# Kernel optimization log

Measured on AMD Instinct MI355X. Metric: run time of the kernel, lower is better.

The kernel has to match this reference:

```python
import jax, jax.numpy as jnp
import numpy as np
import math

B, S, D, H, DFF = 2, 2048, 1024, 16, 4096
DK = D // H
EPS = 1e-5


def setup_inputs() -> dict:
    key = jax.random.key(0)
    ks = jax.random.split(key, 8)
    s = 0.02
    return {
        "x": jax.random.normal(ks[0], (B, S, D), jnp.float32),
        "wq": jax.random.normal(ks[1], (D, D), jnp.float32) * s,
        "bq": jnp.zeros((D,), jnp.float32),
        "wk": jax.random.normal(ks[2], (D, D), jnp.float32) * s,
        "bk": jnp.zeros((D,), jnp.float32),
        "wv": jax.random.normal(ks[3], (D, D), jnp.float32) * s,
        "bv": jnp.zeros((D,), jnp.float32),
        "wo": jax.random.normal(ks[4], (D, D), jnp.float32) * s,
        "bo": jnp.zeros((D,), jnp.float32),
        "g1": jnp.ones((D,), jnp.float32),
        "beta1": jnp.zeros((D,), jnp.float32),
        "w1": jax.random.normal(ks[5], (D, DFF), jnp.float32) * s,
        "b1": jnp.zeros((DFF,), jnp.float32),
        "w2": jax.random.normal(ks[6], (DFF, D), jnp.float32) * s,
        "b2": jnp.zeros((D,), jnp.float32),
        "g2": jnp.ones((D,), jnp.float32),
        "beta2": jnp.zeros((D,), jnp.float32),
    }


def _layernorm(x, g, b):
    m = jnp.mean(x, axis=-1, keepdims=True)
    v = jnp.mean(jnp.square(x - m), axis=-1, keepdims=True)
    return (x - m) * jax.lax.rsqrt(v + EPS) * g + b


def reference(x, wq, bq, wk, bk, wv, bv, wo, bo, g1, beta1, w1, b1, w2, b2, g2, beta2):
    b, s, _ = x.shape
    # QKV projections -> [b, h, s, dk]
    q = (x @ wq + bq).reshape(b, s, H, DK).transpose(0, 2, 1, 3)
    k = (x @ wk + bk).reshape(b, s, H, DK).transpose(0, 2, 1, 3)
    v = (x @ wv + bv).reshape(b, s, H, DK).transpose(0, 2, 1, 3)
    scores = jnp.einsum('bhqd,bhkd->bhqk', q, k) / math.sqrt(DK)  # [b,h,s,s]
    # Faithful to source: softmax over dim=1 (heads axis), not the key axis.
    attn = jax.nn.softmax(scores, axis=1)
    ctx = jnp.einsum('bhqk,bhkd->bhqd', attn, v)
    ctx = ctx.transpose(0, 2, 1, 3).reshape(b, s, D)
    attn_out = ctx @ wo + bo
    # dropout is identity in eval mode
    x1 = _layernorm(x + attn_out, g1, beta1)
    ff = jax.nn.relu(x1 @ w1 + b1) @ w2 + b2
    return _layernorm(x1 + ff, g2, beta2)
```

## Files before the change

kernel.cpp:

```cpp
#include <hip/hip_runtime.h>
#include <stdint.h>

#define B_   2
#define S_   2048
#define D_   1024
#define H_   16
#define DK_  64
#define DFF_ 4096
#define M_   (B_ * S_)
#define QKV_LD 3072

typedef unsigned short u16;
typedef unsigned int   u32;
typedef __attribute__((ext_vector_type(8))) short short8;
typedef __attribute__((ext_vector_type(4))) float f32x4;

__device__ __forceinline__ float b2f(u16 u) {
  union { u32 i; float f; } z; z.i = ((u32)u) << 16; return z.f;
}
__device__ __forceinline__ u16 f2b(float f) {
  union { float f; u32 i; } z; z.f = f;
  u32 x = z.i;
  u32 r = (x + 0x7fffu + ((x >> 16) & 1u)) >> 16;
  return (u16)r;
}
__device__ __forceinline__ void load4(const float* p, float* f) {
  float4 v = *(const float4*)p;
  f[0] = v.x; f[1] = v.y; f[2] = v.z; f[3] = v.w;
}
__device__ __forceinline__ void load4(const u16* p, float* f) {
  uint2 v = *(const uint2*)p;
  f[0] = b2f(v.x & 0xffffu); f[1] = b2f(v.x >> 16);
  f[2] = b2f(v.y & 0xffffu); f[3] = b2f(v.y >> 16);
}
__device__ __forceinline__ void tstore(float* p, float v) { *p = v; }
__device__ __forceinline__ void tstore(u16* p, float v)   { *p = f2b(v); }

__device__ __forceinline__ void gld_lds16(const void* g, void* l) {
  __builtin_amdgcn_global_load_lds(
      (const __attribute__((address_space(1))) void*)g,
      (__attribute__((address_space(3))) void*)l, 16, 0, 0);
}

template<int BM, bool RELU, bool RES, bool BIAS, bool QKV, typename TO>
__global__ __launch_bounds__(256)
void gemm_bf16(const u16* __restrict__ A, const u16* __restrict__ Wt,
               const float* __restrict__ bias0, const float* __restrict__ bias1,
               const float* __restrict__ bias2, const float* __restrict__ res,
               TO* __restrict__ C, int M, int N, int K)
{
  constexpr int WM = BM / 2;
  constexpr int MI = WM / 16;
  __shared__ u16 As[BM][32];
  __shared__ u16 Bs[128][32];

  const int tid  = threadIdx.x;
  const int wave = tid >> 6;
  const int lane = tid & 63;
  const int lo16 = lane & 15;
  const int quad = lane >> 4;
  const int row0 = blockIdx.y * BM;
  const int col0 = blockIdx.x * 128;
  const int mb   = (wave & 1) * WM;
  const int nb   = (wave >> 1) * 64;

  const float* bias = bias0;
  float osc = 1.0f;
  if (QKV) {
    const int seg = col0 >> 10;
    bias = (seg == 0) ? bias0 : (seg == 1 ? bias1 : bias2);
    if (seg == 0) osc = 0.125f;
  }
  const int bc0 = QKV ? (col0 & 1023) : col0;

  f32x4 acc[MI][4];
#pragma unroll
  for (int i = 0; i < MI; ++i)
#pragma unroll
    for (int j = 0; j < 4; ++j) acc[i][j] = (f32x4){0.f, 0.f, 0.f, 0.f};

  const int s_row = tid >> 2;
  const int s_ch  = (tid & 3) * 8;
  const u16* gA = A  + (size_t)(row0 + s_row) * K + s_ch;
  const u16* gB = Wt + (size_t)(col0 + s_row) * K + s_ch;

  for (int k0 = 0; k0 < K; k0 += 32) {
    gld_lds16(gA, &As[s_row][s_ch]);
    if constexpr (BM == 128)
      gld_lds16(gA + (size_t)64 * K, &As[s_row + (BM == 128 ? 64 : 0)][s_ch]);
    gld_lds16(gB, &Bs[s_row][s_ch]);
    gld_lds16(gB + (size_t)64 * K, &Bs[s_row + 64][s_ch]);
    gA += 32; gB += 32;
    __syncthreads();

    short8 af[MI], bf[4];
#pragma unroll
    for (int mi = 0; mi < MI; ++mi)
      af[mi] = *(const short8*)&As[mb + mi * 16 + lo16][quad * 8];
#pragma unroll
    for (int ni = 0; ni < 4; ++ni)
      bf[ni] = *(const short8*)&Bs[nb + ni * 16 + lo16][quad * 8];
#pragma unroll
    for (int mi = 0; mi < MI; ++mi)
#pragma unroll
      for (int ni = 0; ni < 4; ++ni)
        acc[mi][ni] = __builtin_amdgcn_mfma_f32_16x16x32_bf16(af[mi], bf[ni], acc[mi][ni], 0, 0, 0);
    __syncthreads();
  }

  float bv[4];
#pragma unroll
  for (int ni = 0; ni < 4; ++ni)
    bv[ni] = BIAS ? bias[bc0 + nb + ni * 16 + lo16] : 0.f;
#pragma unroll
  for (int mi = 0; mi < MI; ++mi) {
#pragma unroll
    for (int ni = 0; ni < 4; ++ni) {
      const int col = col0 + nb + ni * 16 + lo16;
#pragma unroll
      for (int r = 0; r < 4; ++r) {
        const int row = row0 + mb + mi * 16 + quad * 4 + r;
        float vv = (acc[mi][ni][r] + bv[ni]) * osc;
        if (RELU) vv = fmaxf(vv, 0.f);
        if (RES)  vv += res[(size_t)row * N + col];
        tstore(C + (size_t)row * N + col, vv);
      }
    }
  }
}

__global__ __launch_bounds__(256)
void cvt_f2b(const float* __restrict__ in, u16* __restrict__ out)
{
  const size_t i = ((size_t)blockIdx.x * 256 + threadIdx.x) * 8;
  float4 a = *(const float4*)(in + i);
  float4 b = *(const float4*)(in + i + 4);
  uint4 o;
  o.x = (u32)f2b(a.x) | ((u32)f2b(a.y) << 16);
  o.y = (u32)f2b(a.z) | ((u32)f2b(a.w) << 16);
  o.z = (u32)f2b(b.x) | ((u32)f2b(b.y) << 16);
  o.w = (u32)f2b(b.z) | ((u32)f2b(b.w) << 16);
  *(uint4*)(out + i) = o;
}

__global__ __launch_bounds__(256)
void transpose_f2b(const float* __restrict__ in, u16* __restrict__ out,
                   int ld_in, int ld_out)
{
  __shared__ u16 tile[64][68];
  const int t  = threadIdx.x;
  const int r0 = blockIdx.x * 64;
  const int c0 = blockIdx.y * 64;
  const int rr = t >> 4;
  const int cc = (t & 15) * 4;
#pragma unroll
  for (int rep = 0; rep < 4; ++rep) {
    float4 v = *(const float4*)(in + (size_t)(r0 + rr + rep * 16) * ld_in + c0 + cc);
    tile[rr + rep * 16][cc + 0] = f2b(v.x);
    tile[rr + rep * 16][cc + 1] = f2b(v.y);
    tile[rr + rep * 16][cc + 2] = f2b(v.z);
    tile[rr + rep * 16][cc + 3] = f2b(v.w);
  }
  __syncthreads();
#pragma unroll
  for (int rep = 0; rep < 4; ++rep) {
    const int dr = rr + rep * 16;
    uint2 o;
    o.x = (u32)tile[cc + 0][dr] | ((u32)tile[cc + 1][dr] << 16);
    o.y = (u32)tile[cc + 2][dr] | ((u32)tile[cc + 3][dr] << 16);
    *(uint2*)(out + (size_t)(c0 + dr) * ld_out + r0 + cc) = o;
  }
}

__global__ __launch_bounds__(256)
void transpose_bf16(const u16* __restrict__ in, u16* __restrict__ out,
                    int ld_in, int ld_out)
{
  __shared__ u16 tile[64][68];
  const int t  = threadIdx.x;
  const int r0 = blockIdx.x * 64;
  const int c0 = blockIdx.y * 64;
  const int rr = t >> 4;
  const int cc = (t & 15) * 4;
#pragma unroll
  for (int rep = 0; rep < 4; ++rep) {
    uint2 vv = *(const uint2*)(in + (size_t)(r0 + rr + rep * 16) * ld_in + c0 + cc);
    *(uint2*)&tile[rr + rep * 16][cc] = vv;
  }
  __syncthreads();
#pragma unroll
  for (int rep = 0; rep < 4; ++rep) {
    const int dr = rr + rep * 16;
    uint2 o;
    o.x = (u32)tile[cc + 0][dr] | ((u32)tile[cc + 1][dr] << 16);
    o.y = (u32)tile[cc + 2][dr] | ((u32)tile[cc + 3][dr] << 16);
    *(uint2*)(out + (size_t)(c0 + dr) * ld_out + r0 + cc) = o;
  }
}

__global__ __launch_bounds__(1024)
void attention_mfma(const u16* __restrict__ q, const u16* __restrict__ k,
                    const u16* __restrict__ vt, u16* __restrict__ ctx)
{
  __shared__ __align__(16) u16 Ws[2][16][16][128];

  const int tid  = threadIdx.x;
  const int wave = tid >> 6;
  const int lane = tid & 63;
  const int lo16 = lane & 15;
  const int quad = lane >> 4;

  const int qrow0 = blockIdx.x * 16;
  const int batch = blockIdx.x >> 7;

  if (wave < 8) {
    const int tloc = wave * 16;
    const u16* qrow = q + (size_t)(qrow0 + lo16) * QKV_LD + quad * 8;
    const u16* kbp  = k + (size_t)batch * S_ * QKV_LD;

    for (int s = 0; s < 16; ++s) {
      const int t0 = s * 128;
      u16 (*W)[16][128] = Ws[s & 1];
      const u16* krow = kbp + (size_t)(t0 + tloc + lo16) * QKV_LD + quad * 8;

      f32x4 Sg[16];
#pragma unroll
      for (int h = 0; h < 16; ++h) {
        short8 a0 = *(const short8*)(qrow + h * 64);
        short8 b0 = *(const short8*)(krow + h * 64);
        short8 a1 = *(const short8*)(qrow + h * 64 + 32);
        short8 b1 = *(const short8*)(krow + h * 64 + 32);
        f32x4 sc = (f32x4){0.f, 0.f, 0.f, 0.f};
        sc = __builtin_amdgcn_mfma_f32_16x16x32_bf16(a0, b0, sc, 0, 0, 0);
        sc = __builtin_amdgcn_mfma_f32_16x16x32_bf16(a1, b1, sc, 0, 0, 0);
        Sg[h] = sc;
      }
#pragma unroll
      for (int r = 0; r < 4; ++r) {
        float m = Sg[0][r];
#pragma unroll
        for (int h = 1; h < 16; ++h) m = fmaxf(m, Sg[h][r]);
        float sum = 0.f;
#pragma unroll
        for (int h = 0; h < 16; ++h) {
          float e = __expf(Sg[h][r] - m);
          Sg[h][r] = e;
          sum += e;
        }
        float rinv = 1.0f / sum;
        const int qq  = quad * 4 + r;
        const int pos = (tloc + lo16) ^ ((qq & 7) << 3);
#pragma unroll
        for (int h = 0; h < 16; ++h) {
          union { float f; u32 u; } z; z.f = Sg[h][r] * rinv;
          W[h][qq][pos] = (u16)((z.u + 0x8000u) >> 16);
        }
      }
      __syncthreads();
    }
    __syncthreads();
  } else {
    const int h0 = (wave - 8) * 2;
    f32x4 acc[2][4];
#pragma unroll
    for (int i = 0; i < 2; ++i)
#pragma unroll
      for (int j = 0; j < 4; ++j) acc[i][j] = (f32x4){0.f, 0.f, 0.f, 0.f};

    const u16* vbase[2][4];
#pragma unroll
    for (int hh = 0; hh < 2; ++hh)
#pragma unroll
      for (int dt = 0; dt < 4; ++dt)
        vbase[hh][dt] = vt + (size_t)((h0 + hh) * 64 + dt * 16 + lo16) * M_
                           + (size_t)batch * S_ + quad * 8;

    __syncthreads();
    for (int s = 0; s < 16; ++s) {
      const int t0 = s * 128;
      const u16 (*W)[16][128] = Ws[s & 1];
#pragma unroll
      for (int kc = 0; kc < 4; ++kc) {
        const int kbase = kc * 32 + quad * 8;
        const int ksw   = kbase ^ ((lo16 & 7) << 3);
#pragma unroll
        for (int hh = 0; hh < 2; ++hh) {
          short8 aw = *(const short8*)&W[h0 + hh][lo16][ksw];
#pragma unroll
          for (int dt = 0; dt < 4; ++dt) {
            short8 bv = *(const short8*)(vbase[hh][dt] + t0 + kc * 32);
            acc[hh][dt] = __builtin_amdgcn_mfma_f32_16x16x32_bf16(aw, bv, acc[hh][dt], 0, 0, 0);
          }
        }
      }
      __syncthreads();
    }

    u16* crow = ctx + (size_t)(qrow0 + quad * 4) * D_ + lo16;
#pragma unroll
    for (int hh = 0; hh < 2; ++hh)
#pragma unroll
      for (int dt = 0; dt < 4; ++dt)
#pragma unroll
        for (int r = 0; r < 4; ++r)
          crow[(size_t)r * D_ + (h0 + hh) * 64 + dt * 16] = f2b(acc[hh][dt][r]);
  }
}

__device__ __forceinline__ float block_sum(float vv, float* sm) {
#pragma unroll
  for (int o = 32; o > 0; o >>= 1) vv += __shfl_down(vv, o);
  __syncthreads();
  if ((threadIdx.x & 63) == 0) sm[threadIdx.x >> 6] = vv;
  __syncthreads();
  return sm[0] + sm[1] + sm[2] + sm[3];
}

template<bool HAS_Y, bool AUX>
__global__ __launch_bounds__(256)
void add_ln(const float* __restrict__ x, const u16* __restrict__ y,
            const float* __restrict__ g, const float* __restrict__ bta,
            float* __restrict__ out, u16* __restrict__ aux)
{
  __shared__ float sm[4];
  const int row = blockIdx.x;
  const int t   = threadIdx.x;
  const size_t base = (size_t)row * D_ + t * 4;

  float s[4];
  load4(x + base, s);
  if (HAS_Y) {
    float yv[4];
    load4(y + base, yv);
    s[0] += yv[0]; s[1] += yv[1]; s[2] += yv[2]; s[3] += yv[3];
  }

  float loc = s[0] + s[1] + s[2] + s[3];
  float tot = block_sum(loc, sm);
  float mean = tot * (1.f / 1024.f);
  float d0 = s[0] - mean, d1 = s[1] - mean, d2 = s[2] - mean, d3 = s[3] - mean;
  float sq = d0 * d0 + d1 * d1 + d2 * d2 + d3 * d3;
  float tv = block_sum(sq, sm);
  float rstd = rsqrtf(tv * (1.f / 1024.f) + 1e-5f);

  float4 gv = *(const float4*)(g + t * 4);
  float4 bv = *(const float4*)(bta + t * 4);
  float o0 = d0 * rstd * gv.x + bv.x;
  float o1 = d1 * rstd * gv.y + bv.y;
  float o2 = d2 * rstd * gv.z + bv.z;
  float o3 = d3 * rstd * gv.w + bv.w;
  *(float4*)(out + base) = make_float4(o0, o1, o2, o3);
  if (AUX) {
    uint2 ov;
    ov.x = (u32)f2b(o0) | ((u32)f2b(o1) << 16);
    ov.y = (u32)f2b(o2) | ((u32)f2b(o3) << 16);
    *(uint2*)(aux + base) = ov;
  }
}

extern "C" void kernel_launch(void* const* d_in, const int* in_sizes, int n_in,
                              void* d_out, int out_size, void* d_ws, size_t ws_size,
                              hipStream_t stream) {
  const float* x     = (const float*)d_in[0];
  const float* wq    = (const float*)d_in[1];
  const float* bq    = (const float*)d_in[2];
  const float* wk    = (const float*)d_in[3];
  const float* bk    = (const float*)d_in[4];
  const float* wv    = (const float*)d_in[5];
  const float* bv    = (const float*)d_in[6];
  const float* wo    = (const float*)d_in[7];
  const float* bo    = (const float*)d_in[8];
  const float* g1    = (const float*)d_in[9];
  const float* beta1 = (const float*)d_in[10];
  const float* w1    = (const float*)d_in[11];
  const float* b1    = (const float*)d_in[12];
  const float* w2    = (const float*)d_in[13];
  const float* b2    = (const float*)d_in[14];
  const float* g2    = (const float*)d_in[15];
  const float* beta2 = (const float*)d_in[16];
  float* outF = (float*)d_out;

  char* wsb = (char*)d_ws;
  const size_t MiB = (size_t)1 << 20;
  u16* qkv   = (u16*)(wsb + 0);
  u16* wqkvt = (u16*)(wsb + 24 * MiB);
  u16* vt    = (u16*)(wsb + 24 * MiB);
  u16* ao    = (u16*)(wsb + 8 * MiB);
  u16* wot   = (u16*)(wsb + 16 * MiB);
  u16* x1b   = (u16*)(wsb + 0);
  u16* w1t   = (u16*)(wsb + 8 * MiB);
  u16* w2t   = (u16*)(wsb + 12 * MiB);
  u16* h1    = (u16*)(wsb + 16 * MiB);
  u16* xb    = (u16*)d_out;
  u16* ctx   = (u16*)d_out;
  float* x1  = outF;
  float* z   = outF;

  dim3 blk(256);
  cvt_f2b<<<dim3((M_ * D_) / (256 * 8)), blk, 0, stream>>>(x, xb);
  transpose_f2b<<<dim3(16, 16), blk, 0, stream>>>(wq, wqkvt,                 D_, D_);
  transpose_f2b<<<dim3(16, 16), blk, 0, stream>>>(wk, wqkvt + 1024 * 1024,   D_, D_);
  transpose_f2b<<<dim3(16, 16), blk, 0, stream>>>(wv, wqkvt + 2048 * 1024,   D_, D_);
  gemm_bf16<128, false, false, true, true, u16><<<dim3(QKV_LD / 128, M_ / 128), blk, 0, stream>>>(
      xb, wqkvt, bq, bk, bv, nullptr, qkv, M_, QKV_LD, D_);
  transpose_bf16<<<dim3(M_ / 64, 1024 / 64), blk, 0, stream>>>(qkv + 2048, vt, QKV_LD, M_);
  attention_mfma<<<dim3(M_ / 16), dim3(1024), 0, stream>>>(qkv, qkv + 1024, vt, ctx);
  transpose_f2b<<<dim3(16, 16), blk, 0, stream>>>(wo, wot, D_, D_);
  gemm_bf16<64, false, false, true, false, u16><<<dim3(D_ / 128, M_ / 64), blk, 0, stream>>>(
      ctx, wot, bo, nullptr, nullptr, nullptr, ao, M_, D_, D_);
  add_ln<true, true><<<dim3(M_), blk, 0, stream>>>(x, ao, g1, beta1, x1, x1b);
  transpose_f2b<<<dim3(16, 32), blk, 0, stream>>>(w1, w1t, DFF_, D_);
  transpose_f2b<<<dim3(32, 16), blk, 0, stream>>>(w2, w2t, D_, 2048);
  gemm_bf16<128, true, false, true, false, u16><<<dim3(2048 / 128, M_ / 128), blk, 0, stream>>>(
      x1b, w1t, b1, nullptr, nullptr, nullptr, h1, M_, 2048, D_);
  gemm_bf16<64, false, true, false, false, float><<<dim3(D_ / 128, M_ / 64), blk, 0, stream>>>(
      h1, w2t, nullptr, nullptr, nullptr, x1, z, M_, D_, 2048);
  transpose_f2b<<<dim3(16, 32), blk, 0, stream>>>(w1 + 2048, w1t, DFF_, D_);
  transpose_f2b<<<dim3(32, 16), blk, 0, stream>>>(w2 + (size_t)2048 * 1024, w2t, D_, 2048);
  gemm_bf16<128, true, false, true, false, u16><<<dim3(2048 / 128, M_ / 128), blk, 0, stream>>>(
      x1b, w1t, b1 + 2048, nullptr, nullptr, nullptr, h1, M_, 2048, D_);
  gemm_bf16<64, false, true, true, false, float><<<dim3(D_ / 128, M_ / 64), blk, 0, stream>>>(
      h1, w2t, b2, nullptr, nullptr, z, z, M_, D_, 2048);
  add_ln<false, false><<<dim3(M_), blk, 0, stream>>>(z, nullptr, g2, beta2, outF, nullptr);
}
```

Measured before the change: 685.6 us.

## Split attention key range across blocks with fp32 atomic accumulation

The attention kernel is restructured from a producer/consumer split (8 softmax waves, 8 PV waves, 16 query rows per block) into 512-thread blocks where each block handles 32 query rows over a quarter of the key range. Every wave computes both the head-softmax weights and the PV products, and the block IDs are swizzled. Partial contexts are combined with fp32 atomicAdd into a zeroed buffer, followed by a separate bf16 conversion pass. This is meant to raise occupancy and per-block reuse of V loads, at the cost of an extra memset, atomic traffic, and a conversion kernel.

```diff
diff --git a/kernel.cpp b/kernel.cpp
--- a/kernel.cpp
+++ b/kernel.cpp
@@ -198,11 +198,11 @@
   }
 }
 
-__global__ __launch_bounds__(1024)
+__global__ __launch_bounds__(512, 4)
 void attention_mfma(const u16* __restrict__ q, const u16* __restrict__ k,
-                    const u16* __restrict__ vt, u16* __restrict__ ctx)
-{
-  __shared__ __align__(16) u16 Ws[2][16][16][128];
+                    const u16* __restrict__ vt, float* __restrict__ ctx)
+{
+  __shared__ __align__(16) u16 Ws[16][32][64];
 
   const int tid  = threadIdx.x;
   const int wave = tid >> 6;
@@ -210,19 +210,41 @@
   const int lo16 = lane & 15;
   const int quad = lane >> 4;
 
-  const int qrow0 = blockIdx.x * 16;
-  const int batch = blockIdx.x >> 7;
-
-  if (wave < 8) {
-    const int tloc = wave * 16;
-    const u16* qrow = q + (size_t)(qrow0 + lo16) * QKV_LD + quad * 8;
-    const u16* kbp  = k + (size_t)batch * S_ * QKV_LD;
-
-    for (int s = 0; s < 16; ++s) {
-      const int t0 = s * 128;
-      u16 (*W)[16][128] = Ws[s & 1];
-      const u16* krow = kbp + (size_t)(t0 + tloc + lo16) * QKV_LD + quad * 8;
-
+  const int p = blockIdx.x;
+  const int l = (p & 7) * 64 + (p >> 3);
+  const int quadrant = l >> 6;
+  const int batch = quadrant >> 2;
+  const int chunk = quadrant & 3;
+  const int qt    = l & 63;
+  const int qrow0 = batch * S_ + qt * 32;
+  const int tbase = chunk * 512;
+
+  const int qg = wave >> 2;
+  const int tg = wave & 3;
+  const u16* qrow = q + (size_t)(qrow0 + qg * 16 + lo16) * QKV_LD + quad * 8;
+  const u16* kbp  = k + (size_t)batch * S_ * QKV_LD;
+
+  const int h0 = wave * 2;
+  f32x4 acc[2][2][4];
+#pragma unroll
+  for (int a = 0; a < 2; ++a)
+#pragma unroll
+    for (int b = 0; b < 2; ++b)
+#pragma unroll
+      for (int c = 0; c < 4; ++c) acc[a][b][c] = (f32x4){0.f, 0.f, 0.f, 0.f};
+
+  const u16* vbase[2][4];
+#pragma unroll
+  for (int hh = 0; hh < 2; ++hh)
+#pragma unroll
+    for (int dt = 0; dt < 4; ++dt)
+      vbase[hh][dt] = vt + (size_t)((h0 + hh) * 64 + dt * 16 + lo16) * M_
+                         + (size_t)batch * S_ + tbase + quad * 8;
+
+  for (int s = 0; s < 8; ++s) {
+    {
+      const int t0 = tbase + s * 64;
+      const u16* krow = kbp + (size_t)(t0 + tg * 16 + lo16) * QKV_LD + quad * 8;
       f32x4 Sg[16];
 #pragma unroll
       for (int h = 0; h < 16; ++h) {
@@ -248,63 +270,47 @@
           sum += e;
         }
         float rinv = 1.0f / sum;
-        const int qq  = quad * 4 + r;
-        const int pos = (tloc + lo16) ^ ((qq & 7) << 3);
+        const int qabs = qg * 16 + quad * 4 + r;
+        const int pos  = (tg * 16 + lo16) ^ ((qabs & 7) << 3);
 #pragma unroll
         for (int h = 0; h < 16; ++h) {
           union { float f; u32 u; } z; z.f = Sg[h][r] * rinv;
-          W[h][qq][pos] = (u16)((z.u + 0x8000u) >> 16);
+          Ws[h][qabs][pos] = (u16)((z.u + 0x8000u) >> 16);
         }
       }
-      __syncthreads();
     }
     __syncthreads();
-  } else {
-    const int h0 = (wave - 8) * 2;
-    f32x4 acc[2][4];
-#pragma unroll
-    for (int i = 0; i < 2; ++i)
-#pragma unroll
-      for (int j = 0; j < 4; ++j) acc[i][j] = (f32x4){0.f, 0.f, 0.f, 0.f};
-
-    const u16* vbase[2][4];
-#pragma unroll
-    for (int hh = 0; hh < 2; ++hh)
-#pragma unroll
-      for (int dt = 0; dt < 4; ++dt)
-        vbase[hh][dt] = vt + (size_t)((h0 + hh) * 64 + dt * 16 + lo16) * M_
-                           + (size_t)batch * S_ + quad * 8;
-
-    __syncthreads();
-    for (int s = 0; s < 16; ++s) {
-      const int t0 = s * 128;
-      const u16 (*W)[16][128] = Ws[s & 1];
-#pragma unroll
-      for (int kc = 0; kc < 4; ++kc) {
-        const int kbase = kc * 32 + quad * 8;
-        const int ksw   = kbase ^ ((lo16 & 7) << 3);
-#pragma unroll
-        for (int hh = 0; hh < 2; ++hh) {
-          short8 aw = *(const short8*)&W[h0 + hh][lo16][ksw];
-#pragma unroll
-          for (int dt = 0; dt < 4; ++dt) {
-            short8 bv = *(const short8*)(vbase[hh][dt] + t0 + kc * 32);
-            acc[hh][dt] = __builtin_amdgcn_mfma_f32_16x16x32_bf16(aw, bv, acc[hh][dt], 0, 0, 0);
-          }
+
+#pragma unroll
+    for (int kc = 0; kc < 2; ++kc) {
+      const int ksw = (kc * 32 + quad * 8) ^ ((lo16 & 7) << 3);
+#pragma unroll
+      for (int hh = 0; hh < 2; ++hh) {
+        short8 aw0 = *(const short8*)&Ws[h0 + hh][lo16][ksw];
+        short8 aw1 = *(const short8*)&Ws[h0 + hh][16 + lo16][ksw];
+#pragma unroll
+        for (int dt = 0; dt < 4; ++dt) {
+          short8 bv = *(const short8*)(vbase[hh][dt] + s * 64 + kc * 32);
+          acc[hh][0][dt] = __builtin_amdgcn_mfma_f32_16x16x32_bf16(aw0, bv, acc[hh][0][dt], 0, 0, 0);
+          acc[hh][1][dt] = __builtin_amdgcn_mfma_f32_16x16x32_bf16(aw1, bv, acc[hh][1][dt], 0, 0, 0);
         }
       }
-      __syncthreads();
     }
-
-    u16* crow = ctx + (size_t)(qrow0 + quad * 4) * D_ + lo16;
-#pragma unroll
-    for (int hh = 0; hh < 2; ++hh)
+    __syncthreads();
+  }
+
+#pragma unroll
+  for (int hh = 0; hh < 2; ++hh)
+#pragma unroll
+    for (int qgg = 0; qgg < 2; ++qgg)
 #pragma unroll
       for (int dt = 0; dt < 4; ++dt)
 #pragma unroll
-        for (int r = 0; r < 4; ++r)
-          crow[(size_t)r * D_ + (h0 + hh) * 64 + dt * 16] = f2b(acc[hh][dt][r]);
-  }
+        for (int r = 0; r < 4; ++r) {
+          const int row = qrow0 + qgg * 16 + quad * 4 + r;
+          const int col = (h0 + hh) * 64 + dt * 16 + lo16;
+          atomicAdd(&ctx[(size_t)row * D_ + col], acc[hh][qgg][dt][r]);
+        }
 }
 
 __device__ __forceinline__ float block_sum(float vv, float* sm) {
@@ -385,6 +391,7 @@
   u16* qkv   = (u16*)(wsb + 0);
   u16* wqkvt = (u16*)(wsb + 24 * MiB);
   u16* vt    = (u16*)(wsb + 24 * MiB);
+  u16* ctx_b = (u16*)(wsb + 0);
   u16* ao    = (u16*)(wsb + 8 * MiB);
   u16* wot   = (u16*)(wsb + 16 * MiB);
   u16* x1b   = (u16*)(wsb + 0);
@@ -392,7 +399,7 @@
   u16* w2t   = (u16*)(wsb + 12 * MiB);
   u16* h1    = (u16*)(wsb + 16 * MiB);
   u16* xb    = (u16*)d_out;
-  u16* ctx   = (u16*)d_out;
+  float* ctxF = outF;
   float* x1  = outF;
   float* z   = outF;
 
@@ -404,10 +411,12 @@
   gemm_bf16<128, false, false, true, true, u16><<<dim3(QKV_LD / 128, M_ / 128), blk, 0, stream>>>(
       xb, wqkvt, bq, bk, bv, nullptr, qkv, M_, QKV_LD, D_);
   transpose_bf16<<<dim3(M_ / 64, 1024 / 64), blk, 0, stream>>>(qkv + 2048, vt, QKV_LD, M_);
-  attention_mfma<<<dim3(M_ / 16), dim3(1024), 0, stream>>>(qkv, qkv + 1024, vt, ctx);
+  hipMemsetAsync(d_out, 0, (size_t)M_ * D_ * sizeof(float), stream);
+  attention_mfma<<<dim3(512), dim3(512), 0, stream>>>(qkv, qkv + 1024, vt, ctxF);
+  cvt_f2b<<<dim3((M_ * D_) / (256 * 8)), blk, 0, stream>>>(ctxF, ctx_b);
   transpose_f2b<<<dim3(16, 16), blk, 0, stream>>>(wo, wot, D_, D_);
   gemm_bf16<64, false, false, true, false, u16><<<dim3(D_ / 128, M_ / 64), blk, 0, stream>>>(
-      ctx, wot, bo, nullptr, nullptr, nullptr, ao, M_, D_, D_);
+      ctx_b, wot, bo, nullptr, nullptr, nullptr, ao, M_, D_, D_);
   add_ln<true, true><<<dim3(M_), blk, 0, stream>>>(x, ao, g1, beta1, x1, x1b);
   transpose_f2b<<<dim3(16, 32), blk, 0, stream>>>(w1, w1t, DFF_, D_);
   transpose_f2b<<<dim3(32, 16), blk, 0, stream>>>(w2, w2t, D_, 2048);
```

New measurement: 786.1 us. +14.7%, slower.
